# Performance work log

Measured on AMD Instinct MI355X. Metric: run time of the kernel, lower is better.

The kernel has to match this reference:

```python
import jax, jax.numpy as jnp
import numpy as np

DIM = 1024
NUM_HEADS = 16
HEAD_DIM = DIM // NUM_HEADS


def setup_inputs() -> dict:
    key = jax.random.key(0)
    ks = jax.random.split(key, 8)
    B, N = 4, 1024
    x = jax.random.normal(ks[0], (B, N, DIM), dtype=jnp.float32)
    # RoPE tables per position, broadcast over batch/heads
    pos = jnp.arange(N, dtype=jnp.float32)[:, None]
    inv_freq = 1.0 / (10000.0 ** (jnp.arange(0, HEAD_DIM, 2, dtype=jnp.float32) / HEAD_DIM))
    ang = pos * inv_freq[None, :]                      # [N, D/2]
    ang = jnp.concatenate([ang, ang], axis=-1)          # [N, D]
    cos, sin = jnp.cos(ang), jnp.sin(ang)
    s_in = 1.0 / np.sqrt(DIM)
    qkv_w = jax.random.normal(ks[1], (3 * DIM, DIM), dtype=jnp.float32) * s_in
    qkv_b = jax.random.normal(ks[2], (3 * DIM,), dtype=jnp.float32) * 0.02
    proj_w = jax.random.normal(ks[3], (DIM, DIM), dtype=jnp.float32) * s_in
    proj_b = jax.random.normal(ks[4], (DIM,), dtype=jnp.float32) * 0.02
    return {"x": x, "cos": cos, "sin": sin, "qkv_w": qkv_w, "qkv_b": qkv_b,
            "proj_w": proj_w, "proj_b": proj_b}


def _rotate_half(t):
    t1, t2 = jnp.split(t, 2, axis=-1)
    return jnp.concatenate([-t2, t1], axis=-1)


def reference(x, cos, sin, qkv_w, qkv_b, proj_w, proj_b):
    B, N, C = x.shape
    H, D = NUM_HEADS, HEAD_DIM
    scale = D ** -0.5
    qkv = x @ qkv_w.T + qkv_b                           # [B, N, 3C]
    qkv = qkv.reshape(B, N, 3, H, D).transpose(2, 0, 3, 1, 4)  # [3, B, H, N, D]
    q, k, v = qkv[0], qkv[1], qkv[2]
    q = q * cos + _rotate_half(q) * sin                 # cos/sin [N, D] broadcast
    k = k * cos + _rotate_half(k) * sin
    attn = jnp.einsum('bhnd,bhmd->bhnm', q, k) * scale  # [B, H, N, N]
    attn = jax.nn.softmax(attn, axis=-1)
    out = jnp.einsum('bhnm,bhmd->bhnd', attn, v)        # [B, H, N, D]
    out = out.transpose(0, 2, 1, 3).reshape(B, N, C)
    return out @ proj_w.T + proj_b
```

## Files before the change

kernel.cpp:

```cpp
#include <hip/hip_runtime.h>

typedef __attribute__((ext_vector_type(8))) short bf16x8;
typedef __attribute__((ext_vector_type(4))) float f32x4;
typedef __attribute__((ext_vector_type(4))) unsigned short us4;

#define LOG2E 1.44269504088896f
#define GP(p) (const __attribute__((address_space(1))) void*)(p)
#define LP(p) (__attribute__((address_space(3))) void*)(p)

__device__ inline unsigned short f2bf(float f) {
    unsigned u = __float_as_uint(f);
    u += 0x7fffu + ((u >> 16) & 1u);
    return (unsigned short)(u >> 16);
}

__device__ inline unsigned cvt_pk_bf16(float lo, float hi) {
    unsigned r;
    asm("v_cvt_pk_bf16_f32 %0, %1, %2" : "=v"(r) : "v"(lo), "v"(hi));
    return r;
}

__global__ void cvt3_kernel(const float* __restrict__ x, const float* __restrict__ qw,
                            const float* __restrict__ pw,
                            unsigned short* __restrict__ xb, unsigned short* __restrict__ wqkv,
                            unsigned short* __restrict__ wproj) {
    const int nthreads = gridDim.x * blockDim.x;
    for (int i = blockIdx.x * blockDim.x + threadIdx.x; i < 2097152; i += nthreads) {
        const float* src; unsigned short* dst; int off;
        if (i < 1048576)      { src = x;  dst = xb;    off = i; }
        else if (i < 1835008) { src = qw; dst = wqkv;  off = i - 1048576; }
        else                  { src = pw; dst = wproj; off = i - 1835008; }
        const float4 v = *reinterpret_cast<const float4*>(src + off * 4);
        us4 o;
        o.x = f2bf(v.x); o.y = f2bf(v.y); o.z = f2bf(v.z); o.w = f2bf(v.w);
        *reinterpret_cast<us4*>(dst + off * 4) = o;
    }
}

__device__ inline void gemm_mainloop_db(const unsigned short* __restrict__ A,
                                        const unsigned short* __restrict__ Bw,
                                        unsigned short* As, unsigned short* Bs,
                                        int tm, int tn, f32x4 (&acc)[4][4]) {
    const int K = 1024;
    const int tid = threadIdx.x;
    const int lane = tid & 63;
    const int wv = tid >> 6;
    const int wr = wv >> 1, wc = wv & 1;
    const int lr = lane & 15, lg = lane >> 4;

    const int c1 = tid, c2 = tid + 256;
    const int r1 = c1 >> 2, r2 = c2 >> 2;
    const int g1 = ((c1 & 3) ^ ((r1 >> 1) & 3)) * 8;
    const int g2 = ((c2 & 3) ^ ((r2 >> 1) & 3)) * 8;
    const unsigned short* Ag1 = A + (size_t)(tm * 128 + r1) * K + g1;
    const unsigned short* Ag2 = A + (size_t)(tm * 128 + r2) * K + g2;
    const unsigned short* Bg1 = Bw + (size_t)(tn * 128 + r1) * K + g1;
    const unsigned short* Bg2 = Bw + (size_t)(tn * 128 + r2) * K + g2;

    const int rs = (lr >> 1) & 3;

    auto STAGE = [&](int buf, int k0) {
        __builtin_amdgcn_global_load_lds(GP(Ag1 + k0), LP(As + buf * 4096 + c1 * 8), 16, 0, 0);
        __builtin_amdgcn_global_load_lds(GP(Ag2 + k0), LP(As + buf * 4096 + c2 * 8), 16, 0, 0);
        __builtin_amdgcn_global_load_lds(GP(Bg1 + k0), LP(Bs + buf * 4096 + c1 * 8), 16, 0, 0);
        __builtin_amdgcn_global_load_lds(GP(Bg2 + k0), LP(Bs + buf * 4096 + c2 * 8), 16, 0, 0);
    };

    STAGE(0, 0);
    for (int t = 0; t < 32; t++) {
        const int buf = t & 1;
        if (t < 31) {
            STAGE(buf ^ 1, (t + 1) * 32);
            asm volatile("s_waitcnt vmcnt(4)" ::: "memory");
        } else {
            asm volatile("s_waitcnt vmcnt(0)" ::: "memory");
        }
        __builtin_amdgcn_s_barrier();
        __builtin_amdgcn_sched_barrier(0);

        bf16x8 af[4], bfv[4];
#pragma unroll
        for (int i = 0; i < 4; i++) {
            const int sl = (lg ^ rs) * 8;
            af[i]  = *reinterpret_cast<const bf16x8*>(As + buf * 4096 + (wr * 64 + i * 16 + lr) * 32 + sl);
            bfv[i] = *reinterpret_cast<const bf16x8*>(Bs + buf * 4096 + (wc * 64 + i * 16 + lr) * 32 + sl);
        }
        __builtin_amdgcn_s_setprio(1);
#pragma unroll
        for (int i = 0; i < 4; i++)
#pragma unroll
            for (int j = 0; j < 4; j++)
                acc[i][j] = __builtin_amdgcn_mfma_f32_16x16x32_bf16(af[i], bfv[j], acc[i][j], 0, 0, 0);
        __builtin_amdgcn_s_setprio(0);
        __builtin_amdgcn_s_barrier();
        __builtin_amdgcn_sched_barrier(0);
    }
}

__global__ __launch_bounds__(256, 3) void gemm_qkv_kernel(
        const unsigned short* __restrict__ A, const unsigned short* __restrict__ Bw,
        const float* __restrict__ bias, const float* __restrict__ cosT, const float* __restrict__ sinT,
        unsigned short* __restrict__ Qb, unsigned short* __restrict__ Kb, unsigned short* __restrict__ Vt) {
    __shared__ __align__(16) unsigned short As[2 * 4096];
    __shared__ __align__(16) unsigned short Bs[2 * 4096];
    const int tid = threadIdx.x;
    const int lane = tid & 63;
    const int wv = tid >> 6;
    const int wr = wv >> 1, wc = wv & 1;
    const int tm = blockIdx.y, tn = blockIdx.x;
    const int lr = lane & 15, lg = lane >> 4;

    f32x4 acc[4][4];
#pragma unroll
    for (int i = 0; i < 4; i++)
#pragma unroll
        for (int j = 0; j < 4; j++)
#pragma unroll
            for (int q = 0; q < 4; q++) acc[i][j][q] = 0.f;

    gemm_mainloop_db(A, Bw, As, Bs, tm, tn, acc);

    const int cbase = tn * 128 + wc * 64;
    const int sec = cbase >> 10;
    const int h = (cbase & 1023) >> 6;
    float bias_c[4];
#pragma unroll
    for (int j = 0; j < 4; j++) bias_c[j] = bias[cbase + j * 16 + lr];

    if (sec == 2) {
#pragma unroll
        for (int i = 0; i < 4; i++) {
            const int m0 = tm * 128 + wr * 64 + i * 16 + lg * 4;
            const int b = m0 >> 10, n0 = m0 & 1023;
#pragma unroll
            for (int j = 0; j < 4; j++) {
                const int d = j * 16 + lr;
                us4 pk;
                pk.x = f2bf(acc[i][j][0] + bias_c[j]); pk.y = f2bf(acc[i][j][1] + bias_c[j]);
                pk.z = f2bf(acc[i][j][2] + bias_c[j]); pk.w = f2bf(acc[i][j][3] + bias_c[j]);
                *reinterpret_cast<us4*>(Vt + ((size_t)((b * 16 + h) * 64 + d)) * 1024 + n0) = pk;
            }
        }
    } else {
#pragma unroll
        for (int i = 0; i < 4; i++) {
#pragma unroll
            for (int r = 0; r < 4; r++) {
                const int m = tm * 128 + wr * 64 + i * 16 + lg * 4 + r;
                const int b = m >> 10, n = m & 1023;
                float vals[4];
#pragma unroll
                for (int j = 0; j < 4; j++) vals[j] = acc[i][j][r] + bias_c[j];
#pragma unroll
                for (int j = 0; j < 4; j++) {
                    const int d = j * 16 + lr;
                    const float c = cosT[n * 64 + d];
                    const float s = sinT[n * 64 + d];
                    const float pr = vals[j ^ 2];
                    float outv = vals[j] * c + (d < 32 ? -pr : pr) * s;
                    if (sec == 0) outv *= 0.125f * LOG2E;
                    unsigned short* dst = (sec == 0) ? Qb : Kb;
                    dst[((size_t)((b * 16 + h) * 1024 + n)) * 64 + d] = f2bf(outv);
                }
            }
        }
    }
}

__global__ __launch_bounds__(256, 4) void attn_kernel(
        const unsigned short* __restrict__ Qb, const unsigned short* __restrict__ Kb,
        const unsigned short* __restrict__ Vt, unsigned short* __restrict__ AO) {
    __shared__ __align__(16) unsigned short KVs[2][8192];
    const int tid = threadIdx.x, lane = tid & 63, wv = tid >> 6;
    const int bh = blockIdx.x, qt = blockIdx.y;
    const int qbase = qt * 64 + wv * 16;
    const unsigned short* Qp = Qb + (size_t)bh * 65536;
    const unsigned short* Kp = Kb + (size_t)bh * 65536;
    const unsigned short* Vp = Vt + (size_t)bh * 65536;
    const int lr = lane & 15, lg = lane >> 4;
    const int koff = (lr >> 2) * 8 + (lr & 3);

    const int s1 = tid, s2 = tid + 256;
    const int r1 = s1 >> 3, r2 = s2 >> 3;
    const int sc1 = (s1 & 7) ^ ((r1 & 3) | ((r1 >> 1) & 4));
    const int sc2 = (s2 & 7) ^ ((r2 & 3) | ((r2 >> 1) & 4));
    const unsigned short* Ks1 = Kp + r1 * 64 + sc1 * 8;
    const unsigned short* Ks2 = Kp + r2 * 64 + sc2 * 8;
    const unsigned short* Vs1 = Vp + r1 * 1024 + sc1 * 8;
    const unsigned short* Vs2 = Vp + r2 * 1024 + sc2 * 8;

    auto STAGE = [&](int buf, int kt) {
        unsigned short* base = &KVs[buf][0];
        __builtin_amdgcn_global_load_lds(GP(Ks1 + kt * 64), LP(base + s1 * 8), 16, 0, 0);
        __builtin_amdgcn_global_load_lds(GP(Ks2 + kt * 64), LP(base + s2 * 8), 16, 0, 0);
        __builtin_amdgcn_global_load_lds(GP(Vs1 + kt), LP(base + 4096 + s1 * 8), 16, 0, 0);
        __builtin_amdgcn_global_load_lds(GP(Vs2 + kt), LP(base + 4096 + s2 * 8), 16, 0, 0);
    };

    bf16x8 qfr[2];
#pragma unroll
    for (int kc = 0; kc < 2; kc++)
        qfr[kc] = *reinterpret_cast<const bf16x8*>(Qp + (qbase + lr) * 64 + kc * 32 + lg * 8);

    f32x4 o[4];
    float m_ = -1e30f, l_ = 0.f;
#pragma unroll
    for (int df = 0; df < 4; df++)
#pragma unroll
        for (int r = 0; r < 4; r++) o[df][r] = 0.f;

    auto QK = [&](f32x4 (&s)[4], const unsigned short* Kl) {
#pragma unroll
        for (int kf = 0; kf < 4; kf++)
#pragma unroll
            for (int r = 0; r < 4; r++) s[kf][r] = 0.f;
        __builtin_amdgcn_s_setprio(1);
#pragma unroll
        for (int kc = 0; kc < 2; kc++) {
#pragma unroll
            for (int kf = 0; kf < 4; kf++) {
                const int row = ((kf >> 1) << 5) + ((kf & 1) << 2) + koff;
                const int col = (kc * 4 + lg) ^ ((row & 3) | ((row >> 1) & 4));
                const bf16x8 kfr = *reinterpret_cast<const bf16x8*>(Kl + row * 64 + col * 8);
                s[kf] = __builtin_amdgcn_mfma_f32_16x16x32_bf16(kfr, qfr[kc], s[kf], 0, 0, 0);
            }
        }
        __builtin_amdgcn_s_setprio(0);
    };

    auto SMpack = [&](f32x4 (&s)[4], bf16x8 (&pfr)[2]) {
        float mx = s[0][0];
#pragma unroll
        for (int kf = 0; kf < 4; kf++)
#pragma unroll
            for (int r = 0; r < 4; r++) mx = fmaxf(mx, s[kf][r]);
        if (!__all(mx <= m_ + 11.0f)) {
            mx = fmaxf(mx, __shfl_xor(mx, 16, 64));
            mx = fmaxf(mx, __shfl_xor(mx, 32, 64));
            const float mnew = fmaxf(m_, mx);
            const float fsc = exp2f(m_ - mnew);
            m_ = mnew;
            l_ *= fsc;
#pragma unroll
            for (int df = 0; df < 4; df++)
#pragma unroll
                for (int r = 0; r < 4; r++) o[df][r] *= fsc;
        }
        float rs = 0.f;
#pragma unroll
        for (int kf = 0; kf < 4; kf++)
#pragma unroll
            for (int r = 0; r < 4; r++) {
                const float p = exp2f(s[kf][r] - m_);
                s[kf][r] = p;
                rs += p;
            }
        l_ += rs;
#pragma unroll
        for (int kc = 0; kc < 2; kc++) {
            union { bf16x8 v; unsigned u[4]; } pk;
            pk.u[0] = cvt_pk_bf16(s[2 * kc][0], s[2 * kc][1]);
            pk.u[1] = cvt_pk_bf16(s[2 * kc][2], s[2 * kc][3]);
            pk.u[2] = cvt_pk_bf16(s[2 * kc + 1][0], s[2 * kc + 1][1]);
            pk.u[3] = cvt_pk_bf16(s[2 * kc + 1][2], s[2 * kc + 1][3]);
            pfr[kc] = pk.v;
        }
    };

    auto PV = [&](const unsigned short* Vl, bf16x8 (&pfr)[2]) {
        __builtin_amdgcn_s_setprio(1);
#pragma unroll
        for (int kc = 0; kc < 2; kc++) {
#pragma unroll
            for (int df = 0; df < 4; df++) {
                const int vrow = df * 16 + lr;
                const int vcol = (kc * 4 + lg) ^ ((vrow & 3) | ((vrow >> 1) & 4));
                const bf16x8 vfr = *reinterpret_cast<const bf16x8*>(Vl + vrow * 64 + vcol * 8);
                o[df] = __builtin_amdgcn_mfma_f32_16x16x32_bf16(vfr, pfr[kc], o[df], 0, 0, 0);
            }
        }
        __builtin_amdgcn_s_setprio(0);
    };

    STAGE(0, 0);
    STAGE(1, 64);
    asm volatile("s_waitcnt vmcnt(4)" ::: "memory");
    __builtin_amdgcn_s_barrier();
    __builtin_amdgcn_sched_barrier(0);
    f32x4 sA[4], sB[4];
    QK(sA, &KVs[0][0]);

    bf16x8 pfr[2];
    for (int tt = 0; tt < 8; tt++) {
        SMpack(sA, pfr);
        asm volatile("s_waitcnt vmcnt(0)" ::: "memory");
        __builtin_amdgcn_s_barrier();
        __builtin_amdgcn_sched_barrier(0);
        QK(sB, &KVs[1][0]);
        PV(&KVs[0][4096], pfr);
        __builtin_amdgcn_s_barrier();
        __builtin_amdgcn_sched_barrier(0);
        if (tt < 7) STAGE(0, (2 * tt + 2) * 64);
        SMpack(sB, pfr);
        asm volatile("s_waitcnt vmcnt(0)" ::: "memory");
        __builtin_amdgcn_s_barrier();
        __builtin_amdgcn_sched_barrier(0);
        if (tt < 7) QK(sA, &KVs[0][0]);
        PV(&KVs[1][4096], pfr);
        __builtin_amdgcn_s_barrier();
        __builtin_amdgcn_sched_barrier(0);
        if (tt < 7) STAGE(1, (2 * tt + 3) * 64);
    }

    const int b = bh >> 4, h = bh & 15;
    float lt = l_;
    lt += __shfl_xor(lt, 16, 64);
    lt += __shfl_xor(lt, 32, 64);
    const float rinv = 1.f / lt;
    const int q = qbase + lr;
#pragma unroll
    for (int df = 0; df < 4; df++) {
        us4 pk;
        pk.x = f2bf(o[df][0] * rinv); pk.y = f2bf(o[df][1] * rinv);
        pk.z = f2bf(o[df][2] * rinv); pk.w = f2bf(o[df][3] * rinv);
        *reinterpret_cast<us4*>(AO + (size_t)(b * 1024 + q) * 1024 + h * 64 + df * 16 + lg * 4) = pk;
    }
}

__global__ __launch_bounds__(256, 2) void gemm_proj_kernel(
        const unsigned short* __restrict__ A, const unsigned short* __restrict__ Bw,
        const float* __restrict__ bias, float* __restrict__ out) {
    __shared__ __align__(16) unsigned short As[2 * 8192];
    __shared__ __align__(16) unsigned short Bs[2 * 8192];
    const int tid = threadIdx.x;
    const int lane = tid & 63;
    const int wv = tid >> 6;
    const int wr = wv >> 1, wc = wv & 1;
    const int tm = blockIdx.y, tn = blockIdx.x;
    const int lr = lane & 15, lg = lane >> 4;

    const unsigned short* Ag[4];
    const unsigned short* Bg[4];
    int doff[4];
#pragma unroll
    for (int j = 0; j < 4; j++) {
        const int c = tid + j * 256;
        const int row = c >> 3, sl = c & 7;
        const int gs = (sl ^ ((row & 3) | ((row >> 1) & 4))) * 8;
        Ag[j] = A + (size_t)(tm * 128 + row) * 1024 + gs;
        Bg[j] = Bw + (size_t)(tn * 128 + row) * 1024 + gs;
        doff[j] = c * 8;
    }

    f32x4 acc[4][4];
#pragma unroll
    for (int i = 0; i < 4; i++)
#pragma unroll
        for (int j = 0; j < 4; j++)
#pragma unroll
            for (int q = 0; q < 4; q++) acc[i][j][q] = 0.f;

    auto STAGE = [&](int buf, int k0) {
#pragma unroll
        for (int j = 0; j < 4; j++)
            __builtin_amdgcn_global_load_lds(GP(Ag[j] + k0), LP(As + buf * 8192 + doff[j]), 16, 0, 0);
#pragma unroll
        for (int j = 0; j < 4; j++)
            __builtin_amdgcn_global_load_lds(GP(Bg[j] + k0), LP(Bs + buf * 8192 + doff[j]), 16, 0, 0);
    };

    STAGE(0, 0);
    for (int t = 0; t < 16; t++) {
        const int buf = t & 1;
        if (t < 15) {
            STAGE(buf ^ 1, (t + 1) * 64);
            asm volatile("s_waitcnt vmcnt(8)" ::: "memory");
        } else {
            asm volatile("s_waitcnt vmcnt(0)" ::: "memory");
        }
        __builtin_amdgcn_s_barrier();
        __builtin_amdgcn_sched_barrier(0);

        bf16x8 af[4][2], bfv[4][2];
#pragma unroll
        for (int i = 0; i < 4; i++)
#pragma unroll
            for (int kk = 0; kk < 2; kk++) {
                const int ra = wr * 64 + i * 16 + lr;
                const int rb = wc * 64 + i * 16 + lr;
                af[i][kk]  = *reinterpret_cast<const bf16x8*>(
                    As + buf * 8192 + ra * 64 + ((kk * 4 + lg) ^ ((ra & 3) | ((ra >> 1) & 4))) * 8);
                bfv[i][kk] = *reinterpret_cast<const bf16x8*>(
                    Bs + buf * 8192 + rb * 64 + ((kk * 4 + lg) ^ ((rb & 3) | ((rb >> 1) & 4))) * 8);
            }
        __builtin_amdgcn_s_setprio(1);
#pragma unroll
        for (int i = 0; i < 4; i++)
#pragma unroll
            for (int j = 0; j < 4; j++)
#pragma unroll
                for (int kk = 0; kk < 2; kk++)
                    acc[i][j] = __builtin_amdgcn_mfma_f32_16x16x32_bf16(af[i][kk], bfv[j][kk], acc[i][j], 0, 0, 0);
        __builtin_amdgcn_s_setprio(0);
        __builtin_amdgcn_s_barrier();
        __builtin_amdgcn_sched_barrier(0);
    }

#pragma unroll
    for (int i = 0; i < 4; i++)
#pragma unroll
        for (int j = 0; j < 4; j++)
#pragma unroll
            for (int r = 0; r < 4; r++) {
                const int row = tm * 128 + wr * 64 + i * 16 + lg * 4 + r;
                const int col = tn * 128 + wc * 64 + j * 16 + lr;
                out[(size_t)row * 1024 + col] = acc[i][j][r] + bias[col];
            }
}

extern "C" void kernel_launch(void* const* d_in, const int* in_sizes, int n_in,
                              void* d_out, int out_size, void* d_ws, size_t ws_size,
                              hipStream_t stream) {
    const float* x      = (const float*)d_in[0];
    const float* cosT   = (const float*)d_in[1];
    const float* sinT   = (const float*)d_in[2];
    const float* qkv_w  = (const float*)d_in[3];
    const float* qkv_b  = (const float*)d_in[4];
    const float* proj_w = (const float*)d_in[5];
    const float* proj_b = (const float*)d_in[6];
    float* out = (float*)d_out;

    char* ws = (char*)d_ws;
    unsigned short* xb    = (unsigned short*)(ws);
    unsigned short* wqkv  = (unsigned short*)(ws + (8u << 20));
    unsigned short* wproj = (unsigned short*)(ws + (14u << 20));
    unsigned short* Qb    = (unsigned short*)(ws + (16u << 20));
    unsigned short* Kb    = (unsigned short*)(ws + (24u << 20));
    unsigned short* Vt    = (unsigned short*)(ws + (32u << 20));
    unsigned short* AO    = (unsigned short*)(ws + (40u << 20));

    cvt3_kernel<<<2048, 256, 0, stream>>>(x, qkv_w, proj_w, xb, wqkv, wproj);
    gemm_qkv_kernel<<<dim3(24, 32), 256, 0, stream>>>(xb, wqkv, qkv_b, cosT, sinT, Qb, Kb, Vt);
    attn_kernel<<<dim3(64, 16), 256, 0, stream>>>(Qb, Kb, Vt, AO);
    gemm_proj_kernel<<<dim3(8, 32), 256, 0, stream>>>(AO, wproj, proj_b, out);
}
```

Before: 102.0 us.

## Split K and V staging buffers to deepen attention prefetch pipeline

```diff
diff --git a/kernel.cpp b/kernel.cpp
--- a/kernel.cpp
+++ b/kernel.cpp
@@ -170,7 +170,8 @@
 __global__ __launch_bounds__(256, 4) void attn_kernel(
         const unsigned short* __restrict__ Qb, const unsigned short* __restrict__ Kb,
         const unsigned short* __restrict__ Vt, unsigned short* __restrict__ AO) {
-    __shared__ __align__(16) unsigned short KVs[2][8192];
+    __shared__ __align__(16) unsigned short Kbuf[2][4096];
+    __shared__ __align__(16) unsigned short Vbuf[2][4096];
     const int tid = threadIdx.x, lane = tid & 63, wv = tid >> 6;
     const int bh = blockIdx.x, qt = blockIdx.y;
     const int qbase = qt * 64 + wv * 16;
@@ -189,12 +190,13 @@
     const unsigned short* Vs1 = Vp + r1 * 1024 + sc1 * 8;
     const unsigned short* Vs2 = Vp + r2 * 1024 + sc2 * 8;
 
-    auto STAGE = [&](int buf, int kt) {
-        unsigned short* base = &KVs[buf][0];
-        __builtin_amdgcn_global_load_lds(GP(Ks1 + kt * 64), LP(base + s1 * 8), 16, 0, 0);
-        __builtin_amdgcn_global_load_lds(GP(Ks2 + kt * 64), LP(base + s2 * 8), 16, 0, 0);
-        __builtin_amdgcn_global_load_lds(GP(Vs1 + kt), LP(base + 4096 + s1 * 8), 16, 0, 0);
-        __builtin_amdgcn_global_load_lds(GP(Vs2 + kt), LP(base + 4096 + s2 * 8), 16, 0, 0);
+    auto STAGE_K = [&](int buf, int kt) {
+        __builtin_amdgcn_global_load_lds(GP(Ks1 + kt * 64), LP(&Kbuf[buf][0] + s1 * 8), 16, 0, 0);
+        __builtin_amdgcn_global_load_lds(GP(Ks2 + kt * 64), LP(&Kbuf[buf][0] + s2 * 8), 16, 0, 0);
+    };
+    auto STAGE_V = [&](int buf, int kt) {
+        __builtin_amdgcn_global_load_lds(GP(Vs1 + kt), LP(&Vbuf[buf][0] + s1 * 8), 16, 0, 0);
+        __builtin_amdgcn_global_load_lds(GP(Vs2 + kt), LP(&Vbuf[buf][0] + s2 * 8), 16, 0, 0);
     };
 
     bf16x8 qfr[2];
@@ -282,34 +284,39 @@
         __builtin_amdgcn_s_setprio(0);
     };
 
-    STAGE(0, 0);
-    STAGE(1, 64);
-    asm volatile("s_waitcnt vmcnt(4)" ::: "memory");
+    STAGE_K(0, 0);
+    STAGE_K(1, 64);
+    STAGE_V(0, 0);
+    asm volatile("s_waitcnt vmcnt(0)" ::: "memory");
     __builtin_amdgcn_s_barrier();
     __builtin_amdgcn_sched_barrier(0);
-    f32x4 sA[4], sB[4];
-    QK(sA, &KVs[0][0]);
+    f32x4 sE[4], sO[4];
+    QK(sE, &Kbuf[0][0]);
 
     bf16x8 pfr[2];
+#pragma unroll 1
     for (int tt = 0; tt < 8; tt++) {
-        SMpack(sA, pfr);
-        asm volatile("s_waitcnt vmcnt(0)" ::: "memory");
-        __builtin_amdgcn_s_barrier();
-        __builtin_amdgcn_sched_barrier(0);
-        QK(sB, &KVs[1][0]);
-        PV(&KVs[0][4096], pfr);
-        __builtin_amdgcn_s_barrier();
-        __builtin_amdgcn_sched_barrier(0);
-        if (tt < 7) STAGE(0, (2 * tt + 2) * 64);
-        SMpack(sB, pfr);
-        asm volatile("s_waitcnt vmcnt(0)" ::: "memory");
-        __builtin_amdgcn_s_barrier();
-        __builtin_amdgcn_sched_barrier(0);
-        if (tt < 7) QK(sA, &KVs[0][0]);
-        PV(&KVs[1][4096], pfr);
-        __builtin_amdgcn_s_barrier();
-        __builtin_amdgcn_sched_barrier(0);
-        if (tt < 7) STAGE(1, (2 * tt + 3) * 64);
+        const int t0 = 2 * tt, t1 = 2 * tt + 1;
+        STAGE_K(0, (t0 + 2 < 16 ? t0 + 2 : 15) * 64);
+        STAGE_V(1, t1 * 64);
+        SMpack(sE, pfr);
+        asm volatile("s_waitcnt vmcnt(4)" ::: "memory");
+        __builtin_amdgcn_s_barrier();
+        __builtin_amdgcn_sched_barrier(0);
+        QK(sO, &Kbuf[1][0]);
+        PV(&Vbuf[0][0], pfr);
+        __builtin_amdgcn_s_barrier();
+        __builtin_amdgcn_sched_barrier(0);
+        STAGE_K(1, (t1 + 2 < 16 ? t1 + 2 : 15) * 64);
+        STAGE_V(0, (t1 + 1 < 16 ? t1 + 1 : 15) * 64);
+        SMpack(sO, pfr);
+        asm volatile("s_waitcnt vmcnt(4)" ::: "memory");
+        __builtin_amdgcn_s_barrier();
+        __builtin_amdgcn_sched_barrier(0);
+        if (tt < 7) QK(sE, &Kbuf[0][0]);
+        PV(&Vbuf[1][0], pfr);
+        __builtin_amdgcn_s_barrier();
+        __builtin_amdgcn_sched_barrier(0);
     }
 
     const int b = bh >> 4, h = bh & 15;
```

New measurement: 101.5 us. About the same (-0.4%).
